# Kernel tuning notes

Hardware: AMD Instinct MI355X
Metric: run time of the kernel (lower is better)

## Reference

```python
import jax, jax.numpy as jnp
import numpy as np

EPS = 1e-5  # nn.LayerNorm default eps
N_LAYERS, N, D_IN, H, D_OUT, NH = 4, 2048, 512, 1024, 256, 16


def setup_inputs() -> dict:
    key = jax.random.key(0)
    ks = jax.random.split(key, 8)
    s = lambda k, shape: (jax.random.normal(k, shape, jnp.float32) * 0.02)
    return {
        "x": jax.random.normal(ks[0], (N, D_IN), jnp.float32),
        "W1": s(ks[1], (H, D_IN)), "b1": jnp.zeros((H,), jnp.float32),
        # per-layer MHA params, stacked on a leading layer axis
        "Wqkv": s(ks[2], (N_LAYERS, 3 * H, H)), "bqkv": jnp.zeros((N_LAYERS, 3 * H), jnp.float32),
        "Wo": s(ks[3], (N_LAYERS, H, H)), "bo": jnp.zeros((N_LAYERS, H), jnp.float32),
        "ln_g": jnp.ones((N_LAYERS, H), jnp.float32), "ln_b": jnp.zeros((N_LAYERS, H), jnp.float32),
        "W2": s(ks[4], (D_OUT, H)), "b2": jnp.zeros((D_OUT,), jnp.float32),
        "g_out": jnp.ones((D_OUT,), jnp.float32), "b_out": jnp.zeros((D_OUT,), jnp.float32),
        "num_heads": NH,
    }


def layer_norm(x, g, b):
    m = jnp.mean(x, axis=-1, keepdims=True)
    v = jnp.mean(jnp.square(x - m), axis=-1, keepdims=True)
    return (x - m) * jax.lax.rsqrt(v + EPS) * g + b


def mha(x, Wqkv, bqkv, Wo, bo, nh):
    # x: [N, H]; attention is over the N axis (torch MHA with batch_first=False, batch=1)
    n, h = x.shape
    hd = h // nh
    qkv = x @ Wqkv.T + bqkv                      # [N, 3H]
    q, k, v = jnp.split(qkv, 3, axis=-1)
    q = q.reshape(n, nh, hd).transpose(1, 0, 2)  # [nh, N, hd]
    k = k.reshape(n, nh, hd).transpose(1, 0, 2)
    v = v.reshape(n, nh, hd).transpose(1, 0, 2)
    scale = jnp.float32(1.0 / np.sqrt(hd))
    scores = jnp.einsum('hnd,hmd->hnm', q, k) * scale  # [nh, N, N]
    attn = jax.nn.softmax(scores, axis=-1)
    out = jnp.einsum('hnm,hmd->hnd', attn, v)          # [nh, N, hd]
    out = out.transpose(1, 0, 2).reshape(n, h)
    return out @ Wo.T + bo


def reference(x, W1, b1, Wqkv, bqkv, Wo, bo, ln_g, ln_b, W2, b2, g_out, b_out, num_heads):
    h = jax.nn.relu(x @ W1.T + b1)  # dropout is identity in eval mode
    for i in range(Wqkv.shape[0]):
        a = mha(h, Wqkv[i], bqkv[i], Wo[i], bo[i], num_heads)
        h = layer_norm(a + h, ln_g[i], ln_b[i])
    y = jax.nn.relu(h @ W2.T + b2)
    return layer_norm(y, g_out, b_out)
```

## Files before the change

### kernel.cpp

```cpp
#include <hip/hip_runtime.h>

typedef __attribute__((ext_vector_type(8))) short short8;
typedef __attribute__((ext_vector_type(4))) float f32x4;
typedef __attribute__((ext_vector_type(16))) float f32x16;
typedef __attribute__((ext_vector_type(4))) float float4v;
typedef __attribute__((ext_vector_type(4))) unsigned short ushort4v;
typedef __attribute__((ext_vector_type(4))) unsigned int uint4v;

#define MFMA16(a, b, c) __builtin_amdgcn_mfma_f32_16x16x32_bf16((a), (b), (c), 0, 0, 0)
#define MFMA32(a, b, c) __builtin_amdgcn_mfma_f32_32x32x16_bf16((a), (b), (c), 0, 0, 0)
#define GLOAD_LDS16(g, s)                                                         \
  __builtin_amdgcn_global_load_lds((const __attribute__((address_space(1))) void*)(g), \
                                   (__attribute__((address_space(3))) void*)(s), 16, 0, 0)
#define EXP2(x) __builtin_amdgcn_exp2f(x)

__device__ __forceinline__ unsigned short f2bf(float f) {
  unsigned u = __builtin_bit_cast(unsigned, f);
  u += 0x7fffu + ((u >> 16) & 1u);
  return (unsigned short)(u >> 16);
}

__device__ __forceinline__ unsigned cvtpk(float lo, float hi) {
  unsigned r;
  asm("v_cvt_pk_bf16_f32 %0, %1, %2" : "=v"(r) : "v"(lo), "v"(hi));
  return r;
}

__device__ __forceinline__ void swap32(unsigned& a, unsigned& b) {
  asm volatile("v_permlane32_swap_b32 %0, %1" : "+v"(a), "+v"(b));
}

struct CvtArgs {
  const float* s[5];
  unsigned short* d[5];
  int off[6];
};

__global__ __launch_bounds__(256) void cvt_multi(CvtArgs a, int ntot4) {
  int i4 = blockIdx.x * 256 + threadIdx.x;
  const int stride = gridDim.x * 256;
  for (; i4 < ntot4; i4 += stride) {
    const int idx = i4 * 4;
    int s = 0;
#pragma unroll
    for (int k = 0; k < 4; ++k) s += (idx >= a.off[k + 1]) ? 1 : 0;
    const int local = idx - a.off[s];
    float4v v = *(const float4v*)(a.s[s] + local);
    ushort4v o;
    o.x = f2bf(v.x); o.y = f2bf(v.y); o.z = f2bf(v.z); o.w = f2bf(v.w);
    *(ushort4v*)(a.d[s] + local) = o;
  }
}

template <bool RELU, bool RES, bool OUTF, bool OUTB, bool OUTT>
__global__ __launch_bounds__(256) void gemm_bt(const unsigned short* __restrict__ A,
                                               const unsigned short* __restrict__ B,
                                               const float* __restrict__ bias,
                                               const float* __restrict__ res,
                                               float* __restrict__ outF,
                                               unsigned short* __restrict__ outB,
                                               unsigned short* __restrict__ outT,
                                               int tcol0, int ldt,
                                               int M, int N, int K) {
  __shared__ __align__(16) unsigned short As[2][128 * 32];
  __shared__ __align__(16) unsigned short Bs[2][128 * 32];
  const int tid = threadIdx.x;
  const int w = tid >> 6, lane = tid & 63;
  const int l15 = lane & 15, l4 = lane >> 4;
  const int rowBase = blockIdx.y * 128, colBase = blockIdx.x * 128;
  const int wm = w >> 1, wn = w & 1;

  f32x4 acc[4][4] = {};

  const int c0 = w * 64 + lane;
  const int c1 = 256 + c0;
  const int ra0 = c0 >> 2, ka0 = (c0 & 3) << 3;
  const int ra1 = c1 >> 2, ka1 = (c1 & 3) << 3;

  auto stage = [&](int buf, int k0) {
    GLOAD_LDS16(A + (size_t)(rowBase + ra0) * K + k0 + ka0, As[buf] + w * 512);
    GLOAD_LDS16(A + (size_t)(rowBase + ra1) * K + k0 + ka1, As[buf] + 2048 + w * 512);
    GLOAD_LDS16(B + (size_t)(colBase + ra0) * K + k0 + ka0, Bs[buf] + w * 512);
    GLOAD_LDS16(B + (size_t)(colBase + ra1) * K + k0 + ka1, Bs[buf] + 2048 + w * 512);
  };

  stage(0, 0);
  __syncthreads();

  int p = 0;
  for (int k0 = 0; k0 < K; k0 += 32) {
    if (k0 + 32 < K) stage(p ^ 1, k0 + 32);

    short8 af[4], bf[4];
#pragma unroll
    for (int f = 0; f < 4; ++f) {
      af[f] = *(const short8*)(As[p] + (wm * 64 + f * 16 + l15) * 32 + l4 * 8);
      bf[f] = *(const short8*)(Bs[p] + (wn * 64 + f * 16 + l15) * 32 + l4 * 8);
    }
#pragma unroll
    for (int i = 0; i < 4; ++i)
#pragma unroll
      for (int j = 0; j < 4; ++j)
        acc[i][j] = MFMA16(af[i], bf[j], acc[i][j]);

    __syncthreads();
    p ^= 1;
  }

#pragma unroll
  for (int i = 0; i < 4; ++i) {
    const int row0 = rowBase + wm * 64 + i * 16 + l4 * 4;
#pragma unroll
    for (int j = 0; j < 4; ++j) {
      const int col = colBase + wn * 64 + j * 16 + l15;
      const float bv = bias[col];
      float vv[4];
#pragma unroll
      for (int e = 0; e < 4; ++e) {
        float v = acc[i][j][e] + bv;
        if constexpr (RELU) v = fmaxf(v, 0.f);
        if constexpr (RES) v += res[(size_t)(row0 + e) * N + col];
        vv[e] = v;
        if constexpr (OUTF) outF[(size_t)(row0 + e) * N + col] = v;
        if constexpr (OUTB) outB[(size_t)(row0 + e) * N + col] = f2bf(v);
      }
      if constexpr (OUTT) {
        if (col >= tcol0) {
          ushort4v t;
          t.x = f2bf(vv[0]); t.y = f2bf(vv[1]); t.z = f2bf(vv[2]); t.w = f2bf(vv[3]);
          *(ushort4v*)(outT + (size_t)(col - tcol0) * ldt + row0) = t;
        }
      }
    }
  }
}

__global__ __launch_bounds__(256, 3) void flash_attn4(const unsigned short* __restrict__ qkv,
                                                      const unsigned short* __restrict__ vt,
                                                      float* __restrict__ Op0,
                                                      float* __restrict__ OpR,
                                                      float* __restrict__ Ml,
                                                      float* __restrict__ Ll,
                                                      int Nseq) {
  __shared__ __align__(16) unsigned short Ks[2][64 * 64];
  __shared__ __align__(16) unsigned short Vs[2][64 * 64];
  const int tid = threadIdx.x, w = tid >> 6, lane = tid & 63;
  const int l31 = lane & 31, l2h = lane >> 5, l7 = l31 & 7;
  const float CSC = 0.18033688011112042f;

  const int b = blockIdx.x;
  const int head = (b & 7) * 2 + ((b >> 3) & 1);
  const int s = (b >> 4) & 3;
  const int qb = b >> 6;
  const int q0w = qb * 128 + w * 32;

  const unsigned short* Qp = qkv + head * 64;
  const unsigned short* Kp = qkv + 1024 + head * 64;
  const unsigned short* Vtp = vt + (size_t)head * 64 * Nseq;

  short8 qf[4];
#pragma unroll
  for (int ka = 0; ka < 4; ++ka)
    qf[ka] = *(const short8*)(Qp + (size_t)(q0w + l31) * 3072 + ka * 16 + l2h * 8);

  f32x16 OT0 = {}, OT1 = {};
  float m = -1e30f, ls = 0.f;

  const int sr = tid >> 3, su = tid & 7;
  const int sOffA = sr * 64 + ((su ^ (sr & 7)) * 8);
  const int sOffB = sOffA + 32 * 64;

  const int kt0 = s * (Nseq >> 2);
  const int NIT = Nseq >> 8;

  short8 k0 = *(const short8*)(Kp + (size_t)(kt0 + sr) * 3072 + su * 8);
  short8 k1 = *(const short8*)(Kp + (size_t)(kt0 + sr + 32) * 3072 + su * 8);
  short8 v0 = *(const short8*)(Vtp + (size_t)sr * Nseq + kt0 + su * 8);
  short8 v1 = *(const short8*)(Vtp + (size_t)(sr + 32) * Nseq + kt0 + su * 8);
  *(short8*)(Ks[0] + sOffA) = k0;
  *(short8*)(Ks[0] + sOffB) = k1;
  *(short8*)(Vs[0] + sOffA) = v0;
  *(short8*)(Vs[0] + sOffB) = v1;
  __syncthreads();

  int p = 0;
  for (int it = 0; it < NIT; ++it) {
    const bool more = (it + 1) < NIT;
    if (more) {
      const int ktn = kt0 + (it + 1) * 64;
      k0 = *(const short8*)(Kp + (size_t)(ktn + sr) * 3072 + su * 8);
      k1 = *(const short8*)(Kp + (size_t)(ktn + sr + 32) * 3072 + su * 8);
      v0 = *(const short8*)(Vtp + (size_t)sr * Nseq + ktn + su * 8);
      v1 = *(const short8*)(Vtp + (size_t)(sr + 32) * Nseq + ktn + su * 8);
    }
    const unsigned short* KS = Ks[p];
    const unsigned short* VS = Vs[p];

    f32x16 S0 = {}, S1 = {};
    __builtin_amdgcn_s_setprio(1);
#pragma unroll
    for (int ka = 0; ka < 4; ++ka) {
      const int un = ((ka * 2 + l2h) ^ l7) * 8;
      const short8 a0 = *(const short8*)(KS + l31 * 64 + un);
      const short8 a1 = *(const short8*)(KS + (32 + l31) * 64 + un);
      S0 = MFMA32(a0, qf[ka], S0);
      S1 = MFMA32(a1, qf[ka], S1);
    }
    __builtin_amdgcn_s_setprio(0);

    float pm = S0[0];
#pragma unroll
    for (int r = 1; r < 16; ++r) pm = fmaxf(pm, S0[r]);
#pragma unroll
    for (int r = 0; r < 16; ++r) pm = fmaxf(pm, S1[r]);
    pm = fmaxf(pm, __shfl_xor(pm, 32));
    pm *= CSC;

    if (__any(pm > m + 8.f)) {
      const float mn = fmaxf(m, pm);
      const float fac = EXP2(m - mn);
      m = mn;
      ls *= fac;
#pragma unroll
      for (int r = 0; r < 16; ++r) { OT0[r] *= fac; OT1[r] *= fac; }
    }

    float rs = 0.f;
    unsigned W0[4][2], W1[4][2];
#pragma unroll
    for (int g = 0; g < 4; ++g) {
      const float a0 = EXP2(fmaf(S0[4 * g + 0], CSC, -m));
      const float a1 = EXP2(fmaf(S0[4 * g + 1], CSC, -m));
      const float a2 = EXP2(fmaf(S0[4 * g + 2], CSC, -m));
      const float a3 = EXP2(fmaf(S0[4 * g + 3], CSC, -m));
      const float b0 = EXP2(fmaf(S1[4 * g + 0], CSC, -m));
      const float b1 = EXP2(fmaf(S1[4 * g + 1], CSC, -m));
      const float b2 = EXP2(fmaf(S1[4 * g + 2], CSC, -m));
      const float b3 = EXP2(fmaf(S1[4 * g + 3], CSC, -m));
      rs += ((a0 + a1) + (a2 + a3)) + ((b0 + b1) + (b2 + b3));
      W0[g][0] = cvtpk(a0, a1); W0[g][1] = cvtpk(a2, a3);
      W1[g][0] = cvtpk(b0, b1); W1[g][1] = cvtpk(b2, b3);
    }
    rs += __shfl_xor(rs, 32);
    ls += rs;

    short8 pf[2][2];
#pragma unroll
    for (int ka = 0; ka < 2; ++ka) {
      {
        unsigned x0 = W0[2 * ka][0], y0 = W0[2 * ka + 1][0];
        unsigned x1 = W0[2 * ka][1], y1 = W0[2 * ka + 1][1];
        swap32(x0, y0);
        swap32(x1, y1);
        uint4v u = {x0, x1, y0, y1};
        pf[0][ka] = __builtin_bit_cast(short8, u);
      }
      {
        unsigned x0 = W1[2 * ka][0], y0 = W1[2 * ka + 1][0];
        unsigned x1 = W1[2 * ka][1], y1 = W1[2 * ka + 1][1];
        swap32(x0, y0);
        swap32(x1, y1);
        uint4v u = {x0, x1, y0, y1};
        pf[1][ka] = __builtin_bit_cast(short8, u);
      }
    }

    __builtin_amdgcn_s_setprio(1);
#pragma unroll
    for (int sub = 0; sub < 2; ++sub)
#pragma unroll
      for (int ka = 0; ka < 2; ++ka) {
        const int un = ((sub * 4 + ka * 2 + l2h) ^ l7) * 8;
        const short8 va0 = *(const short8*)(VS + l31 * 64 + un);
        const short8 va1 = *(const short8*)(VS + (32 + l31) * 64 + un);
        OT0 = MFMA32(va0, pf[sub][ka], OT0);
        OT1 = MFMA32(va1, pf[sub][ka], OT1);
      }
    __builtin_amdgcn_s_setprio(0);

    if (more) {
      unsigned short* Kn = Ks[p ^ 1];
      unsigned short* Vn = Vs[p ^ 1];
      *(short8*)(Kn + sOffA) = k0;
      *(short8*)(Kn + sOffB) = k1;
      *(short8*)(Vn + sOffA) = v0;
      *(short8*)(Vn + sOffB) = v1;
    }
    __syncthreads();
    p ^= 1;
  }

  float* Ob = (s == 0) ? Op0 : (OpR + (size_t)(s - 1) * Nseq * 1024);
  const int q = q0w + l31;
#pragma unroll
  for (int g = 0; g < 4; ++g) {
    const int d0 = 8 * g + 4 * l2h;
    float4v t0 = {OT0[4 * g], OT0[4 * g + 1], OT0[4 * g + 2], OT0[4 * g + 3]};
    float4v t1 = {OT1[4 * g], OT1[4 * g + 1], OT1[4 * g + 2], OT1[4 * g + 3]};
    *(float4v*)(Ob + (size_t)q * 1024 + head * 64 + d0) = t0;
    *(float4v*)(Ob + (size_t)q * 1024 + head * 64 + 32 + d0) = t1;
  }
  if (l2h == 0) {
    Ml[(size_t)(s * 16 + head) * Nseq + q] = m;
    Ll[(size_t)(s * 16 + head) * Nseq + q] = ls;
  }
}

__global__ __launch_bounds__(256) void attn_combine4(const float* __restrict__ Op0,
                                                     const float* __restrict__ OpR,
                                                     const float* __restrict__ Ml,
                                                     const float* __restrict__ Ll,
                                                     unsigned short* __restrict__ out, int Nseq) {
  const int t = blockIdx.x * 256 + threadIdx.x;
  const int q = t >> 8, c4 = (t & 255) * 4;
  const int head = c4 >> 6;
  float mm[4], lv[4];
  float M = -1e30f;
#pragma unroll
  for (int s = 0; s < 4; ++s) {
    mm[s] = Ml[(size_t)(s * 16 + head) * Nseq + q];
    lv[s] = Ll[(size_t)(s * 16 + head) * Nseq + q];
    M = fmaxf(M, mm[s]);
  }
  float denom = 0.f;
  float4v acc = {0.f, 0.f, 0.f, 0.f};
#pragma unroll
  for (int s = 0; s < 4; ++s) {
    const float ww = EXP2(mm[s] - M);
    denom += lv[s] * ww;
    const float* Ob = (s == 0) ? Op0 : (OpR + (size_t)(s - 1) * Nseq * 1024);
    float4v o = *(const float4v*)(Ob + (size_t)q * 1024 + c4);
    acc.x += o.x * ww; acc.y += o.y * ww; acc.z += o.z * ww; acc.w += o.w * ww;
  }
  const float inv = 1.f / denom;
  ushort4v r;
  r.x = f2bf(acc.x * inv);
  r.y = f2bf(acc.y * inv);
  r.z = f2bf(acc.z * inv);
  r.w = f2bf(acc.w * inv);
  *(ushort4v*)(out + (size_t)q * 1024 + c4) = r;
}

template <int D>
__global__ __launch_bounds__(256) void ln_rows(const float* __restrict__ src,
                                               const float* __restrict__ gw,
                                               const float* __restrict__ bw,
                                               float* __restrict__ outF,
                                               unsigned short* __restrict__ outB) {
  __shared__ float red[4];
  const int row = blockIdx.x;
  const int tid = threadIdx.x, w = tid >> 6;
  constexpr int PT = D / 256;
  const float* r = src + (size_t)row * D;
  float v[PT];
  float s = 0.f;
#pragma unroll
  for (int i = 0; i < PT; ++i) { v[i] = r[tid + i * 256]; s += v[i]; }
#pragma unroll
  for (int off = 32; off; off >>= 1) s += __shfl_down(s, off);
  if ((tid & 63) == 0) red[w] = s;
  __syncthreads();
  const float mean = (red[0] + red[1] + red[2] + red[3]) / D;
  __syncthreads();
  float q = 0.f;
#pragma unroll
  for (int i = 0; i < PT; ++i) { const float d = v[i] - mean; q += d * d; }
#pragma unroll
  for (int off = 32; off; off >>= 1) q += __shfl_down(q, off);
  if ((tid & 63) == 0) red[w] = q;
  __syncthreads();
  const float rstd = rsqrtf((red[0] + red[1] + red[2] + red[3]) / D + 1e-5f);
#pragma unroll
  for (int i = 0; i < PT; ++i) {
    const int c = tid + i * 256;
    const float o = (v[i] - mean) * rstd * gw[c] + bw[c];
    outF[(size_t)row * D + c] = o;
    if (outB) outB[(size_t)row * D + c] = f2bf(o);
  }
}

extern "C" void kernel_launch(void* const* d_in, const int* in_sizes, int n_in,
                              void* d_out, int out_size, void* d_ws, size_t ws_size,
                              hipStream_t stream) {
  const int N = 2048, D_IN = 512, H = 1024, D_OUT = 256, NL = 4;
  const float* x    = (const float*)d_in[0];
  const float* W1   = (const float*)d_in[1];
  const float* b1   = (const float*)d_in[2];
  const float* Wqkv = (const float*)d_in[3];
  const float* bqkv = (const float*)d_in[4];
  const float* Wo   = (const float*)d_in[5];
  const float* bo   = (const float*)d_in[6];
  const float* lng  = (const float*)d_in[7];
  const float* lnb  = (const float*)d_in[8];
  const float* W2   = (const float*)d_in[9];
  const float* b2   = (const float*)d_in[10];
  const float* gout = (const float*)d_in[11];
  const float* bout = (const float*)d_in[12];
  float* out = (float*)d_out;

  char* ws = (char*)d_ws;
  auto alloc = [&](size_t bytes) -> char* {
    char* p = ws;
    ws += (bytes + 255) & ~(size_t)255;
    return p;
  };
  unsigned short* xb    = (unsigned short*)alloc((size_t)N * D_IN * 2);
  unsigned short* W1b   = (unsigned short*)alloc((size_t)H * D_IN * 2);
  unsigned short* Wqkvb = (unsigned short*)alloc((size_t)NL * 3 * H * H * 2);
  unsigned short* Wob   = (unsigned short*)alloc((size_t)NL * H * H * 2);
  unsigned short* W2b   = (unsigned short*)alloc((size_t)D_OUT * H * 2);
  unsigned short* hb    = (unsigned short*)alloc((size_t)N * H * 2);
  unsigned short* qkvb  = (unsigned short*)alloc((size_t)N * 3 * H * 2);
  unsigned short* aob   = (unsigned short*)alloc((size_t)N * H * 2);
  unsigned short* vtg   = (unsigned short*)alloc((size_t)H * N * 2);
  float* hf  = (float*)alloc((size_t)N * H * 4);
  float* af  = (float*)alloc((size_t)N * H * 4);
  float* opR = (float*)alloc((size_t)3 * N * H * 4);
  float* ml  = (float*)alloc((size_t)4 * 16 * N * 4);
  float* ll  = (float*)alloc((size_t)4 * 16 * N * 4);
  float* yf  = (float*)alloc((size_t)N * D_OUT * 4);
  float* op0 = af;

  CvtArgs ca;
  ca.s[0] = x;    ca.d[0] = xb;
  ca.s[1] = W1;   ca.d[1] = W1b;
  ca.s[2] = Wqkv; ca.d[2] = Wqkvb;
  ca.s[3] = Wo;   ca.d[3] = Wob;
  ca.s[4] = W2;   ca.d[4] = W2b;
  const int n0 = N * D_IN, n1 = H * D_IN, n2 = NL * 3 * H * H, n3 = NL * H * H, n4 = D_OUT * H;
  ca.off[0] = 0;
  ca.off[1] = n0;
  ca.off[2] = n0 + n1;
  ca.off[3] = n0 + n1 + n2;
  ca.off[4] = n0 + n1 + n2 + n3;
  ca.off[5] = n0 + n1 + n2 + n3 + n4;
  const int ntot4 = ca.off[5] / 4;
  cvt_multi<<<2048, 256, 0, stream>>>(ca, ntot4);

  gemm_bt<true, false, true, true, false><<<dim3(H / 128, N / 128), 256, 0, stream>>>(
      xb, W1b, b1, nullptr, hf, hb, nullptr, 0, 0, N, H, D_IN);

  for (int l = 0; l < NL; ++l) {
    gemm_bt<false, false, false, true, true><<<dim3(3 * H / 128, N / 128), 256, 0, stream>>>(
        hb, Wqkvb + (size_t)l * 3 * H * H, bqkv + (size_t)l * 3 * H, nullptr, nullptr, qkvb,
        vtg, 2 * H, N, N, 3 * H, H);
    flash_attn4<<<1024, 256, 0, stream>>>(qkvb, vtg, op0, opR, ml, ll, N);
    attn_combine4<<<(N * H / 4) / 256, 256, 0, stream>>>(op0, opR, ml, ll, aob, N);
    gemm_bt<false, true, true, false, false><<<dim3(H / 128, N / 128), 256, 0, stream>>>(
        aob, Wob + (size_t)l * H * H, bo + (size_t)l * H, hf, af, nullptr, nullptr, 0, 0,
        N, H, H);
    ln_rows<1024><<<N, 256, 0, stream>>>(af, lng + (size_t)l * H, lnb + (size_t)l * H, hf, hb);
  }

  gemm_bt<true, false, true, false, false><<<dim3(D_OUT / 128, N / 128), 256, 0, stream>>>(
      hb, W2b, b2, nullptr, yf, nullptr, nullptr, 0, 0, N, D_OUT, H);
  ln_rows<256><<<N, 256, 0, stream>>>(yf, gout, bout, out, nullptr);
}
```

Before: 423.3 us.

## Template GEMM tile sizes, remap blocks across XCDs, store attention partials in bf16

The GEMM kernel is templated on tile size so the smaller GEMMs (W1, Wo, W2) use 128x64 or 64x64 tiles. This launches more workgroups on a GPU with many compute units. A 1D grid with an XCD-aware block remapping replaces the 2D grid, grouping neighbouring tiles for cache locality. Flash-attention split partial outputs are now stored in bf16 instead of fp32, halving the write and read traffic of the combine step, at some cost in precision of the unnormalized partial sums.

```diff
diff --git a/kernel.cpp b/kernel.cpp
--- a/kernel.cpp
+++ b/kernel.cpp
@@ -6,6 +6,7 @@
 typedef __attribute__((ext_vector_type(4))) float float4v;
 typedef __attribute__((ext_vector_type(4))) unsigned short ushort4v;
 typedef __attribute__((ext_vector_type(4))) unsigned int uint4v;
+typedef __attribute__((ext_vector_type(2))) unsigned int uint2v;
 
 #define MFMA16(a, b, c) __builtin_amdgcn_mfma_f32_16x16x32_bf16((a), (b), (c), 0, 0, 0)
 #define MFMA32(a, b, c) __builtin_amdgcn_mfma_f32_32x32x16_bf16((a), (b), (c), 0, 0, 0)
@@ -30,6 +31,13 @@
   asm volatile("v_permlane32_swap_b32 %0, %1" : "+v"(a), "+v"(b));
 }
 
+__device__ __forceinline__ float bflo(unsigned u) {
+  return __builtin_bit_cast(float, u << 16);
+}
+__device__ __forceinline__ float bfhi(unsigned u) {
+  return __builtin_bit_cast(float, u & 0xffff0000u);
+}
+
 struct CvtArgs {
   const float* s[5];
   unsigned short* d[5];
@@ -52,7 +60,7 @@
   }
 }
 
-template <bool RELU, bool RES, bool OUTF, bool OUTB, bool OUTT>
+template <int BM, int BN, bool RELU, bool RES, bool OUTF, bool OUTB, bool OUTT>
 __global__ __launch_bounds__(256) void gemm_bt(const unsigned short* __restrict__ A,
                                                const unsigned short* __restrict__ B,
                                                const float* __restrict__ bias,
@@ -62,26 +70,35 @@
                                                unsigned short* __restrict__ outT,
                                                int tcol0, int ldt,
                                                int M, int N, int K) {
-  __shared__ __align__(16) unsigned short As[2][128 * 32];
-  __shared__ __align__(16) unsigned short Bs[2][128 * 32];
+  __shared__ __align__(16) unsigned short As[2][BM * 32];
+  __shared__ __align__(16) unsigned short Bs[2][BN * 32];
+  constexpr int MI = BM / 32, MJ = BN / 32, CA = BM / 64, CB = BN / 64;
   const int tid = threadIdx.x;
   const int w = tid >> 6, lane = tid & 63;
   const int l15 = lane & 15, l4 = lane >> 4;
-  const int rowBase = blockIdx.y * 128, colBase = blockIdx.x * 128;
+
+  const int nwg = gridDim.x;
+  const int wg = (blockIdx.x & 7) * (nwg >> 3) + (blockIdx.x >> 3);
+  const int nbx = N / BN;
+  const int rowBase = (wg / nbx) * BM;
+  const int colBase = (wg % nbx) * BN;
   const int wm = w >> 1, wn = w & 1;
 
-  f32x4 acc[4][4] = {};
-
-  const int c0 = w * 64 + lane;
-  const int c1 = 256 + c0;
-  const int ra0 = c0 >> 2, ka0 = (c0 & 3) << 3;
-  const int ra1 = c1 >> 2, ka1 = (c1 & 3) << 3;
+  f32x4 acc[MI][MJ] = {};
 
   auto stage = [&](int buf, int k0) {
-    GLOAD_LDS16(A + (size_t)(rowBase + ra0) * K + k0 + ka0, As[buf] + w * 512);
-    GLOAD_LDS16(A + (size_t)(rowBase + ra1) * K + k0 + ka1, As[buf] + 2048 + w * 512);
-    GLOAD_LDS16(B + (size_t)(colBase + ra0) * K + k0 + ka0, Bs[buf] + w * 512);
-    GLOAD_LDS16(B + (size_t)(colBase + ra1) * K + k0 + ka1, Bs[buf] + 2048 + w * 512);
+#pragma unroll
+    for (int i = 0; i < CA; ++i) {
+      const int c = i * 256 + tid;
+      GLOAD_LDS16(A + (size_t)(rowBase + (c >> 2)) * K + k0 + ((c & 3) << 3),
+                  As[buf] + i * 2048 + w * 512);
+    }
+#pragma unroll
+    for (int i = 0; i < CB; ++i) {
+      const int c = i * 256 + tid;
+      GLOAD_LDS16(B + (size_t)(colBase + (c >> 2)) * K + k0 + ((c & 3) << 3),
+                  Bs[buf] + i * 2048 + w * 512);
+    }
   };
 
   stage(0, 0);
@@ -91,16 +108,17 @@
   for (int k0 = 0; k0 < K; k0 += 32) {
     if (k0 + 32 < K) stage(p ^ 1, k0 + 32);
 
-    short8 af[4], bf[4];
-#pragma unroll
-    for (int f = 0; f < 4; ++f) {
-      af[f] = *(const short8*)(As[p] + (wm * 64 + f * 16 + l15) * 32 + l4 * 8);
-      bf[f] = *(const short8*)(Bs[p] + (wn * 64 + f * 16 + l15) * 32 + l4 * 8);
-    }
-#pragma unroll
-    for (int i = 0; i < 4; ++i)
-#pragma unroll
-      for (int j = 0; j < 4; ++j)
+    short8 af[MI], bf[MJ];
+#pragma unroll
+    for (int f = 0; f < MI; ++f)
+      af[f] = *(const short8*)(As[p] + (wm * (BM / 2) + f * 16 + l15) * 32 + l4 * 8);
+#pragma unroll
+    for (int f = 0; f < MJ; ++f)
+      bf[f] = *(const short8*)(Bs[p] + (wn * (BN / 2) + f * 16 + l15) * 32 + l4 * 8);
+#pragma unroll
+    for (int i = 0; i < MI; ++i)
+#pragma unroll
+      for (int j = 0; j < MJ; ++j)
         acc[i][j] = MFMA16(af[i], bf[j], acc[i][j]);
 
     __syncthreads();
@@ -108,11 +126,11 @@
   }
 
 #pragma unroll
-  for (int i = 0; i < 4; ++i) {
-    const int row0 = rowBase + wm * 64 + i * 16 + l4 * 4;
-#pragma unroll
-    for (int j = 0; j < 4; ++j) {
-      const int col = colBase + wn * 64 + j * 16 + l15;
+  for (int i = 0; i < MI; ++i) {
+    const int row0 = rowBase + wm * (BM / 2) + i * 16 + l4 * 4;
+#pragma unroll
+    for (int j = 0; j < MJ; ++j) {
+      const int col = colBase + wn * (BN / 2) + j * 16 + l15;
       const float bv = bias[col];
       float vv[4];
 #pragma unroll
@@ -137,8 +155,8 @@
 
 __global__ __launch_bounds__(256, 3) void flash_attn4(const unsigned short* __restrict__ qkv,
                                                       const unsigned short* __restrict__ vt,
-                                                      float* __restrict__ Op0,
-                                                      float* __restrict__ OpR,
+                                                      unsigned short* __restrict__ Op0,
+                                                      unsigned short* __restrict__ OpR,
                                                       float* __restrict__ Ml,
                                                       float* __restrict__ Ll,
                                                       int Nseq) {
@@ -290,15 +308,15 @@
     p ^= 1;
   }
 
-  float* Ob = (s == 0) ? Op0 : (OpR + (size_t)(s - 1) * Nseq * 1024);
+  unsigned short* Ob = (s == 0) ? Op0 : (OpR + (size_t)(s - 1) * Nseq * 1024);
   const int q = q0w + l31;
 #pragma unroll
   for (int g = 0; g < 4; ++g) {
     const int d0 = 8 * g + 4 * l2h;
-    float4v t0 = {OT0[4 * g], OT0[4 * g + 1], OT0[4 * g + 2], OT0[4 * g + 3]};
-    float4v t1 = {OT1[4 * g], OT1[4 * g + 1], OT1[4 * g + 2], OT1[4 * g + 3]};
-    *(float4v*)(Ob + (size_t)q * 1024 + head * 64 + d0) = t0;
-    *(float4v*)(Ob + (size_t)q * 1024 + head * 64 + 32 + d0) = t1;
+    uint2v t0 = {cvtpk(OT0[4 * g], OT0[4 * g + 1]), cvtpk(OT0[4 * g + 2], OT0[4 * g + 3])};
+    uint2v t1 = {cvtpk(OT1[4 * g], OT1[4 * g + 1]), cvtpk(OT1[4 * g + 2], OT1[4 * g + 3])};
+    *(uint2v*)(Ob + (size_t)q * 1024 + head * 64 + d0) = t0;
+    *(uint2v*)(Ob + (size_t)q * 1024 + head * 64 + 32 + d0) = t1;
   }
   if (l2h == 0) {
     Ml[(size_t)(s * 16 + head) * Nseq + q] = m;
@@ -306,8 +324,8 @@
   }
 }
 
-__global__ __launch_bounds__(256) void attn_combine4(const float* __restrict__ Op0,
-                                                     const float* __restrict__ OpR,
+__global__ __launch_bounds__(256) void attn_combine4(const unsigned short* __restrict__ Op0,
+                                                     const unsigned short* __restrict__ OpR,
                                                      const float* __restrict__ Ml,
                                                      const float* __restrict__ Ll,
                                                      unsigned short* __restrict__ out, int Nseq) {
@@ -328,9 +346,12 @@
   for (int s = 0; s < 4; ++s) {
     const float ww = EXP2(mm[s] - M);
     denom += lv[s] * ww;
-    const float* Ob = (s == 0) ? Op0 : (OpR + (size_t)(s - 1) * Nseq * 1024);
-    float4v o = *(const float4v*)(Ob + (size_t)q * 1024 + c4);
-    acc.x += o.x * ww; acc.y += o.y * ww; acc.z += o.z * ww; acc.w += o.w * ww;
+    const unsigned short* Ob = (s == 0) ? Op0 : (OpR + (size_t)(s - 1) * Nseq * 1024);
+    uint2v o = *(const uint2v*)(Ob + (size_t)q * 1024 + c4);
+    acc.x += bflo(o.x) * ww;
+    acc.y += bfhi(o.x) * ww;
+    acc.z += bflo(o.y) * ww;
+    acc.w += bfhi(o.y) * ww;
   }
   const float inv = 1.f / denom;
   ushort4v r;
@@ -413,13 +434,13 @@
   unsigned short* qkvb  = (unsigned short*)alloc((size_t)N * 3 * H * 2);
   unsigned short* aob   = (unsigned short*)alloc((size_t)N * H * 2);
   unsigned short* vtg   = (unsigned short*)alloc((size_t)H * N * 2);
+  unsigned short* opb0  = (unsigned short*)alloc((size_t)N * H * 2);
+  unsigned short* opbR  = (unsigned short*)alloc((size_t)3 * N * H * 2);
   float* hf  = (float*)alloc((size_t)N * H * 4);
   float* af  = (float*)alloc((size_t)N * H * 4);
-  float* opR = (float*)alloc((size_t)3 * N * H * 4);
   float* ml  = (float*)alloc((size_t)4 * 16 * N * 4);
   float* ll  = (float*)alloc((size_t)4 * 16 * N * 4);
   float* yf  = (float*)alloc((size_t)N * D_OUT * 4);
-  float* op0 = af;
 
   CvtArgs ca;
   ca.s[0] = x;    ca.d[0] = xb;
@@ -437,22 +458,22 @@
   const int ntot4 = ca.off[5] / 4;
   cvt_multi<<<2048, 256, 0, stream>>>(ca, ntot4);
 
-  gemm_bt<true, false, true, true, false><<<dim3(H / 128, N / 128), 256, 0, stream>>>(
+  gemm_bt<128, 64, true, false, true, true, false><<<(N / 128) * (H / 64), 256, 0, stream>>>(
       xb, W1b, b1, nullptr, hf, hb, nullptr, 0, 0, N, H, D_IN);
 
   for (int l = 0; l < NL; ++l) {
-    gemm_bt<false, false, false, true, true><<<dim3(3 * H / 128, N / 128), 256, 0, stream>>>(
+    gemm_bt<128, 128, false, false, false, true, true><<<(N / 128) * (3 * H / 128), 256, 0, stream>>>(
         hb, Wqkvb + (size_t)l * 3 * H * H, bqkv + (size_t)l * 3 * H, nullptr, nullptr, qkvb,
         vtg, 2 * H, N, N, 3 * H, H);
-    flash_attn4<<<1024, 256, 0, stream>>>(qkvb, vtg, op0, opR, ml, ll, N);
-    attn_combine4<<<(N * H / 4) / 256, 256, 0, stream>>>(op0, opR, ml, ll, aob, N);
-    gemm_bt<false, true, true, false, false><<<dim3(H / 128, N / 128), 256, 0, stream>>>(
+    flash_attn4<<<1024, 256, 0, stream>>>(qkvb, vtg, opb0, opbR, ml, ll, N);
+    attn_combine4<<<(N * H / 4) / 256, 256, 0, stream>>>(opb0, opbR, ml, ll, aob, N);
+    gemm_bt<128, 64, false, true, true, false, false><<<(N / 128) * (H / 64), 256, 0, stream>>>(
         aob, Wob + (size_t)l * H * H, bo + (size_t)l * H, hf, af, nullptr, nullptr, 0, 0,
         N, H, H);
     ln_rows<1024><<<N, 256, 0, stream>>>(af, lng + (size_t)l * H, lnb + (size_t)l * H, hf, hb);
   }
 
-  gemm_bt<true, false, true, false, false><<<dim3(D_OUT / 128, N / 128), 256, 0, stream>>>(
+  gemm_bt<64, 64, true, false, true, false, false><<<(N / 64) * (D_OUT / 64), 256, 0, stream>>>(
       hb, W2b, b2, nullptr, yf, nullptr, nullptr, 0, 0, N, D_OUT, H);
   ln_rows<256><<<N, 256, 0, stream>>>(yf, gout, bout, out, nullptr);
 }
```

Result: no change. 417.0 us (-1.5%).
